# Kernel optimization log

Measured on AMD Instinct MI355X. Metric: run time of the kernel, lower is better.

The kernel has to match this reference:

```python
import jax, jax.numpy as jnp
import numpy as np

N_NODES = 50000
N_EDGES = 800000
N_GRAPHS = 256
F_IN, HID, EMB = 128, 256, 128
N_GROUPS, N_FAM = 16, 128


def setup_inputs() -> dict:
    key = jax.random.key(0)
    ks = jax.random.split(key, 12)
    x = jax.random.normal(ks[0], (N_NODES, F_IN), dtype=jnp.float32)
    edge_index = jax.random.randint(ks[1], (2, N_EDGES), 0, N_NODES, dtype=jnp.int64)
    batch = jnp.sort(jax.random.randint(ks[2], (N_NODES,), 0, N_GRAPHS, dtype=jnp.int64))
    def lin(k, fi, fo):
        s = 1.0 / np.sqrt(fi)
        return jax.random.uniform(k, (fi, fo), minval=-s, maxval=s, dtype=jnp.float32)
    W1 = lin(ks[3], F_IN, HID); b1 = jnp.zeros((HID,), jnp.float32)
    W2 = lin(ks[4], HID, EMB); b2 = jnp.zeros((EMB,), jnp.float32)
    Wg = lin(ks[5], EMB, N_GROUPS); bg = jnp.zeros((N_GROUPS,), jnp.float32)
    s = 1.0 / np.sqrt(EMB)
    Wf = jax.random.uniform(ks[6], (N_GROUPS, EMB, N_FAM), minval=-s, maxval=s, dtype=jnp.float32)
    bf = jnp.zeros((N_GROUPS, N_FAM), jnp.float32)
    return {"x": x, "edge_index": edge_index, "batch": batch,
            "W1": W1, "b1": b1, "W2": W2, "b2": b2,
            "Wg": Wg, "bg": bg, "Wf": Wf, "bf": bf}


def _gcn_conv(h, src, dst, coef, W, b, n):
    # h: [N, Fin]; src/dst: [E'] (self-loops included); coef: [E'] sym-norm
    hw = h @ W                                    # [N, Fout]
    msg = hw[src] * coef[:, None]                 # gather + scale, [E', Fout]
    out = jax.ops.segment_sum(msg, dst, num_segments=n)  # scatter-add
    return out + b


def reference(x, edge_index, batch, W1, b1, W2, b2, Wg, bg, Wf, bf):
    n = x.shape[0]
    loops = jnp.arange(n, dtype=edge_index.dtype)
    src = jnp.concatenate([edge_index[0], loops])
    dst = jnp.concatenate([edge_index[1], loops])
    # symmetric GCN normalization (deg >= 1 thanks to self-loops)
    deg = jax.ops.segment_sum(jnp.ones_like(dst, dtype=x.dtype), dst, num_segments=n)
    dinv = jax.lax.rsqrt(deg)
    coef = dinv[src] * dinv[dst]

    h1 = jax.nn.relu(_gcn_conv(x, src, dst, coef, W1, b1, n))  # dropout = identity (eval)
    h2 = _gcn_conv(h1, src, dst, coef, W2, b2, n)

    # global mean pool over graphs
    sums = jax.ops.segment_sum(h2, batch, num_segments=N_GRAPHS)
    cnts = jax.ops.segment_sum(jnp.ones((n,), x.dtype), batch, num_segments=N_GRAPHS)
    embeddings = sums / jnp.maximum(cnts, 1.0)[:, None]        # [G, EMB]

    group_logits = embeddings @ Wg + bg                        # [G, n_groups]
    pred_groups = jnp.argmax(group_logits, axis=1)             # routing
    # per-graph routed family classifier (dense equivalent of the dict outputs)
    family_logits = jnp.einsum('gd,gdf->gf', embeddings, Wf[pred_groups]) + bf[pred_groups]
    return embeddings, group_logits, family_logits
```

## Files before the change

kernel.cpp:

```cpp
#include <hip/hip_runtime.h>
#include <hip/hip_fp16.h>
#include <cstddef>
#include <cstdint>

static constexpr int NN   = 50000;
static constexpr int NE   = 800000;
static constexpr int NG   = 256;
static constexpr int FIN  = 128;
static constexpr int HID  = 256;
static constexpr int EMB  = 128;
static constexpr int NGRP = 16;
static constexpr int NFAM = 128;
static constexpr int NETOT = NE + NN;

static constexpr int SCAN_B  = 256;
static constexpr int SCAN_CH = (NN + SCAN_B - 1) / SCAN_B;

using bf16x8 = __attribute__((ext_vector_type(8))) short;
using f32x4  = __attribute__((ext_vector_type(4))) float;

__device__ __forceinline__ unsigned short f2bf(float f) {
    uint32_t u = __float_as_uint(f);
    u += 0x7FFFu + ((u >> 16) & 1u);
    return (unsigned short)(u >> 16);
}
__device__ __forceinline__ float bf2f(unsigned short u) {
    return __uint_as_float((uint32_t)u << 16);
}
__device__ __forceinline__ uint32_t pack_sw(int s, float w) {
    return (uint32_t)s | ((uint32_t)__half_as_ushort(__float2half(w)) << 16);
}
__device__ __forceinline__ void unpack_sw(uint32_t v, int& s, float& w) {
    s = (int)(v & 0xFFFFu);
    w = __half2float(__ushort_as_half((unsigned short)(v >> 16)));
}


__global__ void k_init_deg(int* __restrict__ degi, int n) {
    int i = blockIdx.x * blockDim.x + threadIdx.x;
    if (i < n) degi[i] = 1;
}

__global__ void k_count(const int* __restrict__ edst, int* __restrict__ degi, int e) {
    int i = blockIdx.x * blockDim.x + threadIdx.x;
    if (i < e) atomicAdd(degi + edst[i], 1);
}

__global__ void k_prep(const int* __restrict__ degi, const int* __restrict__ batch,
                       float* __restrict__ dinv, int* __restrict__ gstart,
                       float* __restrict__ pooled, int n, int G) {
    int i = blockIdx.x * blockDim.x + threadIdx.x;
    if (i < NG * HID) pooled[i] = 0.f;
    if (i >= n) return;
    dinv[i] = rsqrtf((float)degi[i]);
    int b  = batch[i];
    int pb = (i == 0) ? -1 : batch[i - 1];
    for (int g = pb + 1; g <= b; ++g) gstart[g] = i;
    if (i == n - 1) {
        for (int g = b + 1; g <= G; ++g) gstart[g] = n;
    }
}

__global__ void k_xconv(const float* __restrict__ x, unsigned short* __restrict__ xb) {
    size_t i = (size_t)(blockIdx.x * blockDim.x + threadIdx.x) * 8;
    float4 a = *(const float4*)(x + i);
    float4 b = *(const float4*)(x + i + 4);
    uint4 o;
    o.x = (uint32_t)f2bf(a.x) | ((uint32_t)f2bf(a.y) << 16);
    o.y = (uint32_t)f2bf(a.z) | ((uint32_t)f2bf(a.w) << 16);
    o.z = (uint32_t)f2bf(b.x) | ((uint32_t)f2bf(b.y) << 16);
    o.w = (uint32_t)f2bf(b.z) | ((uint32_t)f2bf(b.w) << 16);
    *(uint4*)(xb + i) = o;
}

__global__ void k_w1t(const float* __restrict__ W1, unsigned short* __restrict__ W1t) {
    int t = blockIdx.x * blockDim.x + threadIdx.x;
    int nidx = t >> 7, k = t & 127;
    W1t[t] = f2bf(W1[(size_t)k * HID + nidx]);
}


__global__ __launch_bounds__(256) void k_scanA(const int* __restrict__ degi,
                                               int* __restrict__ row_ptr,
                                               int* __restrict__ bsum, int n) {
    __shared__ int sh[256];
    const int b = blockIdx.x, t = threadIdx.x;
    const int idx = b * SCAN_CH + t;
    int v = 0;
    if (t < SCAN_CH && idx < n) v = degi[idx];
    sh[t] = v;
    __syncthreads();
    for (int off = 1; off < 256; off <<= 1) {
        int y = (t >= off) ? sh[t - off] : 0;
        __syncthreads();
        if (t >= off) sh[t] += y;
        __syncthreads();
    }
    if (t < SCAN_CH && idx < n) row_ptr[idx] = sh[t] - v;
    if (t == 255) bsum[b] = sh[255];
}

__global__ __launch_bounds__(256) void k_scanB(const int* __restrict__ bsum,
                                               const int* __restrict__ gstart,
                                               float* __restrict__ rcnt,
                                               int* __restrict__ row_ptr,
                                               int* __restrict__ cursor, int n) {
    __shared__ int sh[SCAN_B];
    const int b = blockIdx.x, t = threadIdx.x;
    sh[t] = bsum[t];
    __syncthreads();
    for (int off = 1; off < SCAN_B; off <<= 1) {
        int y = (t >= off) ? sh[t - off] : 0;
        __syncthreads();
        if (t >= off) sh[t] += y;
        __syncthreads();
    }
    const int boff = (b == 0) ? 0 : sh[b - 1];
    const int idx  = b * SCAN_CH + t;
    if (t < SCAN_CH && idx < n) {
        row_ptr[idx] += boff;
        cursor[idx] = 1;
    }
    if (b == 0 && t == 0) row_ptr[n] = sh[SCAN_B - 1];
    if (b == 0 && t < NG) {
        int c = gstart[t + 1] - gstart[t];
        rcnt[t] = 1.0f / (float)max(c, 1);
    }
}

__global__ void k_build(const int* __restrict__ esrc, const int* __restrict__ edst,
                        const int* __restrict__ batch, const float* __restrict__ dinv,
                        const float* __restrict__ rcnt, const int* __restrict__ row_ptr,
                        int* __restrict__ cursor, uint32_t* __restrict__ eA,
                        uint32_t* __restrict__ eP, int n, int e) {
    int i = blockIdx.x * blockDim.x + threadIdx.x;
    if (i < n) {
        int p = row_ptr[i];
        float di = dinv[i];
        eA[p] = pack_sw(i, di);
        eP[p] = pack_sw(i, di * di * rcnt[batch[i]]);
    } else if (i < n + e) {
        int ei = i - n;
        int d = edst[ei], s = esrc[ei];
        int p = atomicAdd(cursor + d, 1);
        int idx = row_ptr[d] + p;
        float ds = dinv[s];
        eA[idx] = pack_sw(s, ds);
        eP[idx] = pack_sw(s, dinv[d] * ds * rcnt[batch[d]]);
    }
}


__global__ __launch_bounds__(256) void k_agg(
        const unsigned short* __restrict__ xb, const int* __restrict__ row_ptr,
        const uint32_t* __restrict__ eA, const float* __restrict__ dinv,
        unsigned short* __restrict__ xa, int n) {
    int node = blockIdx.x * 4 + (threadIdx.x >> 6);
    if (node >= n) return;
    int lane = threadIdx.x & 63;
    int grp = lane >> 4, fl = lane & 15;
    float acc[8] = {};
    int beg = row_ptr[node], end = row_ptr[node + 1];
    for (int j = beg; j < end; j += 4) {
        int jj = j + grp;
        bool valid = jj < end;
        uint32_t ev = __builtin_nontemporal_load(eA + (valid ? jj : beg));
        int s; float w;
        unpack_sw(ev, s, w);
        if (!valid) w = 0.f;
        bf16x8 v = *(const bf16x8*)(xb + ((size_t)s << 7) + fl * 8);
#pragma unroll
        for (int k = 0; k < 8; ++k)
            acc[k] += w * bf2f((unsigned short)v[k]);
    }
#pragma unroll
    for (int k = 0; k < 8; ++k) {
        acc[k] += __shfl_xor(acc[k], 16);
        acc[k] += __shfl_xor(acc[k], 32);
    }
    if (lane < 16) {
        float di = dinv[node];
        uint4 o;
        o.x = (uint32_t)f2bf(di * acc[0]) | ((uint32_t)f2bf(di * acc[1]) << 16);
        o.y = (uint32_t)f2bf(di * acc[2]) | ((uint32_t)f2bf(di * acc[3]) << 16);
        o.z = (uint32_t)f2bf(di * acc[4]) | ((uint32_t)f2bf(di * acc[5]) << 16);
        o.w = (uint32_t)f2bf(di * acc[6]) | ((uint32_t)f2bf(di * acc[7]) << 16);
        *(uint4*)(xa + ((size_t)node << 7) + fl * 8) = o;
    }
}


__global__ __launch_bounds__(256) void k_gemm_mfma(
        const unsigned short* __restrict__ A, const unsigned short* __restrict__ Bt,
        const float* __restrict__ bias, unsigned short* __restrict__ C, int M) {
    const int m0 = blockIdx.x * 64;
    const int w  = threadIdx.x >> 6;
    const int l  = threadIdx.x & 63;
    const int lr = l & 15;
    const int lk = l >> 4;
    const int n0 = blockIdx.y * 64 + w * 16;

    f32x4 acc[4] = {};
#pragma unroll
    for (int ks = 0; ks < 4; ++ks) {
        const int k0 = ks * 32;
        bf16x8 bfr = *(const bf16x8*)(Bt + (size_t)(n0 + lr) * FIN + k0 + lk * 8);
#pragma unroll
        for (int mi = 0; mi < 4; ++mi) {
            int row = m0 + mi * 16 + lr;
            row = min(row, M - 1);
            bf16x8 afr = *(const bf16x8*)(A + ((size_t)row << 7) + k0 + lk * 8);
            acc[mi] = __builtin_amdgcn_mfma_f32_16x16x32_bf16(afr, bfr, acc[mi], 0, 0, 0);
        }
    }
    float b = bias[n0 + lr];
#pragma unroll
    for (int mi = 0; mi < 4; ++mi) {
#pragma unroll
        for (int r = 0; r < 4; ++r) {
            int row = m0 + mi * 16 + lk * 4 + r;
            if (row < M) {
                float v = fmaxf(acc[mi][r] + b, 0.f);
                C[(size_t)row * HID + n0 + lr] = f2bf(v);
            }
        }
    }
}


__global__ __launch_bounds__(256) void k_pool(
        const unsigned short* __restrict__ h1, const int* __restrict__ row_ptr,
        const int* __restrict__ gstart, const uint32_t* __restrict__ eP,
        float* __restrict__ pooled) {
    __shared__ float red[4][HID];
    const int g  = blockIdx.x >> 3;
    const int kb = blockIdx.x & 7;
    const int e0 = row_ptr[gstart[g]];
    const int e1 = row_ptr[gstart[g + 1]];
    const int len = e1 - e0;
    const int per = (len + 7) >> 3;
    const int s0  = e0 + kb * per;
    const int s1  = min(s0 + per, e1);
    const int lane = threadIdx.x & 63;
    const int wv   = threadIdx.x >> 6;
    const int half = lane >> 5, fl = lane & 31;

    float acc[8] = {};
    for (int j = s0 + wv * 2; j < s1; j += 8) {
        int jj = j + half;
        bool valid = jj < s1;
        uint32_t ev = __builtin_nontemporal_load(eP + (valid ? jj : s0));
        int s; float w;
        unpack_sw(ev, s, w);
        if (!valid) w = 0.f;
        bf16x8 v = *(const bf16x8*)(h1 + ((size_t)s << 8) + fl * 8);
#pragma unroll
        for (int k = 0; k < 8; ++k)
            acc[k] += w * bf2f((unsigned short)v[k]);
    }
#pragma unroll
    for (int k = 0; k < 8; ++k)
        acc[k] += __shfl_xor(acc[k], 32);
    if (lane < 32) {
#pragma unroll
        for (int k = 0; k < 8; ++k)
            red[wv][fl * 8 + k] = acc[k];
    }
    __syncthreads();
    int t = threadIdx.x;
    float v = red[0][t] + red[1][t] + red[2][t] + red[3][t];
    if (v != 0.f) atomicAdd(&pooled[g * HID + t], v);
}


__global__ __launch_bounds__(128) void k_head(const float* __restrict__ pooled,
                                              const float* __restrict__ W2,
                                              const float* __restrict__ b2,
                                              const float* __restrict__ Wg,
                                              const float* __restrict__ bg,
                                              const float* __restrict__ Wf,
                                              const float* __restrict__ bf,
                                              float* __restrict__ out_emb,
                                              float* __restrict__ out_gl,
                                              float* __restrict__ out_fl) {
    __shared__ float p[HID];
    __shared__ float e[EMB];
    __shared__ float gl[NGRP];
    __shared__ int ps;
    int g = blockIdx.x, c = threadIdx.x;
    for (int i = c; i < HID; i += 128) p[i] = pooled[(size_t)g * HID + i];
    __syncthreads();
    float a = b2[c];
    for (int k = 0; k < HID; ++k) a += p[k] * W2[(size_t)k * EMB + c];
    e[c] = a;
    out_emb[(size_t)g * EMB + c] = a;
    __syncthreads();
    if (c < NGRP) {
        float s = bg[c];
        for (int d = 0; d < EMB; ++d) s += e[d] * Wg[d * NGRP + c];
        gl[c] = s;
        out_gl[g * NGRP + c] = s;
    }
    __syncthreads();
    if (c == 0) {
        int bi = 0;
        float bv = gl[0];
        for (int t2 = 1; t2 < NGRP; ++t2)
            if (gl[t2] > bv) { bv = gl[t2]; bi = t2; }
        ps = bi;
    }
    __syncthreads();
    int pr = ps;
    float s = bf[pr * NFAM + c];
    for (int d = 0; d < EMB; ++d) s += e[d] * Wf[((size_t)pr * EMB + d) * NFAM + c];
    out_fl[g * NFAM + c] = s;
}


extern "C" void kernel_launch(void* const* d_in, const int* in_sizes, int n_in,
                              void* d_out, int out_size, void* d_ws, size_t ws_size,
                              hipStream_t stream) {
    const float* x   = (const float*)d_in[0];
    const int*   ei  = (const int*)d_in[1];
    const int*   bat = (const int*)d_in[2];
    const float* W1  = (const float*)d_in[3];
    const float* b1  = (const float*)d_in[4];
    const float* W2  = (const float*)d_in[5];
    const float* b2  = (const float*)d_in[6];
    const float* Wg  = (const float*)d_in[7];
    const float* bg  = (const float*)d_in[8];
    const float* Wf  = (const float*)d_in[9];
    const float* bf  = (const float*)d_in[10];

    float* out     = (float*)d_out;
    float* out_emb = out;
    float* out_gl  = out + (size_t)NG * EMB;
    float* out_fl  = out_gl + (size_t)NG * NGRP;

    char* w = (char*)d_ws;
    auto alloc = [&](size_t bytes) {
        char* p = w;
        w += (bytes + 255) & ~(size_t)255;
        return p;
    };
    int*            degi    = (int*)alloc((size_t)NN * 4);
    float*          dinv    = (float*)alloc((size_t)NN * 4);
    int*            row_ptr = (int*)alloc((size_t)(NN + 1) * 4);
    int*            cursor  = (int*)alloc((size_t)NN * 4);
    int*            bsum    = (int*)alloc((size_t)SCAN_B * 4);
    uint32_t*       eA      = (uint32_t*)alloc((size_t)NETOT * 4);
    uint32_t*       eP      = (uint32_t*)alloc((size_t)NETOT * 4);
    int*            gstart  = (int*)alloc((size_t)(NG + 1) * 4);
    float*          rcnt    = (float*)alloc((size_t)NG * 4);
    unsigned short* xb      = (unsigned short*)alloc((size_t)NN * FIN * 2);
    unsigned short* xa      = (unsigned short*)alloc((size_t)NN * FIN * 2);
    unsigned short* W1t     = (unsigned short*)alloc((size_t)HID * FIN * 2);
    unsigned short* h1      = (unsigned short*)alloc((size_t)NN * HID * 2);
    float*          pooled  = (float*)alloc((size_t)NG * HID * 4);

    const int* esrc = ei;
    const int* edst = ei + NE;

    k_init_deg<<<(NN + 255) / 256, 256, 0, stream>>>(degi, NN);
    k_count<<<(NE + 255) / 256, 256, 0, stream>>>(edst, degi, NE);
    k_prep<<<(NG * HID + 255) / 256, 256, 0, stream>>>(degi, bat, dinv, gstart,
                                                       pooled, NN, NG);
    k_xconv<<<(NN * FIN / 8 + 255) / 256, 256, 0, stream>>>(x, xb);
    k_w1t<<<(HID * FIN + 255) / 256, 256, 0, stream>>>(W1, W1t);
    k_scanA<<<SCAN_B, 256, 0, stream>>>(degi, row_ptr, bsum, NN);
    k_scanB<<<SCAN_B, 256, 0, stream>>>(bsum, gstart, rcnt, row_ptr, cursor, NN);
    k_build<<<(NETOT + 255) / 256, 256, 0, stream>>>(esrc, edst, bat, dinv, rcnt,
                                                     row_ptr, cursor, eA, eP, NN, NE);

    k_agg<<<(NN + 3) / 4, 256, 0, stream>>>(xb, row_ptr, eA, dinv, xa, NN);
    {
        dim3 grid((NN + 63) / 64, HID / 64);
        k_gemm_mfma<<<grid, 256, 0, stream>>>(xa, W1t, b1, h1, NN);
    }

    k_pool<<<NG * 8, 256, 0, stream>>>(h1, row_ptr, gstart, eP, pooled);

    k_head<<<NG, 128, 0, stream>>>(pooled, W2, b2, Wg, bg, Wf, bf,
                                   out_emb, out_gl, out_fl);
}
```

Baseline: 258.6 us.

## Fuse second GCN linear into first GEMM and pool over 128-wide features

The second layer's W2 projection now runs inside the first GEMM kernel: each 64-row block computes relu(xa@W1+b1), keeps it in swizzled LDS, multiplies by W2, and writes a 128-wide H. This replaces the 256-wide h1 intermediate and the per-graph W2 matvec in the head. The source-side dinv scaling is folded into x before aggregation and into H, so edge lists store only indices or dst-side weights. The trade-offs are an extra bf16 rounding of h1 before the second GEMM, 32KB of LDS per block that may limit occupancy, and a bias b2 that is added only for nonempty graphs.

```diff
diff --git a/kernel.cpp b/kernel.cpp
--- a/kernel.cpp
+++ b/kernel.cpp
@@ -48,9 +48,9 @@
 
 __global__ void k_prep(const int* __restrict__ degi, const int* __restrict__ batch,
                        float* __restrict__ dinv, int* __restrict__ gstart,
-                       float* __restrict__ pooled, int n, int G) {
+                       float* __restrict__ emb_acc, int n, int G) {
     int i = blockIdx.x * blockDim.x + threadIdx.x;
-    if (i < NG * HID) pooled[i] = 0.f;
+    if (i < NG * EMB) emb_acc[i] = 0.f;
     if (i >= n) return;
     dinv[i] = rsqrtf((float)degi[i]);
     int b  = batch[i];
@@ -61,22 +61,31 @@
     }
 }
 
-__global__ void k_xconv(const float* __restrict__ x, unsigned short* __restrict__ xb) {
-    size_t i = (size_t)(blockIdx.x * blockDim.x + threadIdx.x) * 8;
+__global__ void k_xconv(const float* __restrict__ x, const float* __restrict__ dinv,
+                        unsigned short* __restrict__ xs) {
+    int t = blockIdx.x * blockDim.x + threadIdx.x;
+    size_t i = (size_t)t * 8;
+    float dv = dinv[t >> 4];
     float4 a = *(const float4*)(x + i);
     float4 b = *(const float4*)(x + i + 4);
     uint4 o;
-    o.x = (uint32_t)f2bf(a.x) | ((uint32_t)f2bf(a.y) << 16);
-    o.y = (uint32_t)f2bf(a.z) | ((uint32_t)f2bf(a.w) << 16);
-    o.z = (uint32_t)f2bf(b.x) | ((uint32_t)f2bf(b.y) << 16);
-    o.w = (uint32_t)f2bf(b.z) | ((uint32_t)f2bf(b.w) << 16);
-    *(uint4*)(xb + i) = o;
+    o.x = (uint32_t)f2bf(dv * a.x) | ((uint32_t)f2bf(dv * a.y) << 16);
+    o.y = (uint32_t)f2bf(dv * a.z) | ((uint32_t)f2bf(dv * a.w) << 16);
+    o.z = (uint32_t)f2bf(dv * b.x) | ((uint32_t)f2bf(dv * b.y) << 16);
+    o.w = (uint32_t)f2bf(dv * b.z) | ((uint32_t)f2bf(dv * b.w) << 16);
+    *(uint4*)(xs + i) = o;
 }
 
 __global__ void k_w1t(const float* __restrict__ W1, unsigned short* __restrict__ W1t) {
     int t = blockIdx.x * blockDim.x + threadIdx.x;
     int nidx = t >> 7, k = t & 127;
     W1t[t] = f2bf(W1[(size_t)k * HID + nidx]);
+}
+
+__global__ void k_w2t(const float* __restrict__ W2, unsigned short* __restrict__ W2t) {
+    int t = blockIdx.x * blockDim.x + threadIdx.x;
+    int nidx = t >> 8, k = t & 255;
+    W2t[t] = f2bf(W2[(size_t)k * EMB + nidx]);
 }
 
 
@@ -131,29 +140,27 @@
 __global__ void k_build(const int* __restrict__ esrc, const int* __restrict__ edst,
                         const int* __restrict__ batch, const float* __restrict__ dinv,
                         const float* __restrict__ rcnt, const int* __restrict__ row_ptr,
-                        int* __restrict__ cursor, uint32_t* __restrict__ eA,
+                        int* __restrict__ cursor, int* __restrict__ eA,
                         uint32_t* __restrict__ eP, int n, int e) {
     int i = blockIdx.x * blockDim.x + threadIdx.x;
     if (i < n) {
         int p = row_ptr[i];
-        float di = dinv[i];
-        eA[p] = pack_sw(i, di);
-        eP[p] = pack_sw(i, di * di * rcnt[batch[i]]);
+        eA[p] = i;
+        eP[p] = pack_sw(i, dinv[i] * rcnt[batch[i]]);
     } else if (i < n + e) {
         int ei = i - n;
         int d = edst[ei], s = esrc[ei];
         int p = atomicAdd(cursor + d, 1);
         int idx = row_ptr[d] + p;
-        float ds = dinv[s];
-        eA[idx] = pack_sw(s, ds);
-        eP[idx] = pack_sw(s, dinv[d] * ds * rcnt[batch[d]]);
+        eA[idx] = s;
+        eP[idx] = pack_sw(s, dinv[d] * rcnt[batch[d]]);
     }
 }
 
 
 __global__ __launch_bounds__(256) void k_agg(
-        const unsigned short* __restrict__ xb, const int* __restrict__ row_ptr,
-        const uint32_t* __restrict__ eA, const float* __restrict__ dinv,
+        const unsigned short* __restrict__ xs, const int* __restrict__ row_ptr,
+        const int* __restrict__ eA, const float* __restrict__ dinv,
         unsigned short* __restrict__ xa, int n) {
     int node = blockIdx.x * 4 + (threadIdx.x >> 6);
     if (node >= n) return;
@@ -164,14 +171,12 @@
     for (int j = beg; j < end; j += 4) {
         int jj = j + grp;
         bool valid = jj < end;
-        uint32_t ev = __builtin_nontemporal_load(eA + (valid ? jj : beg));
-        int s; float w;
-        unpack_sw(ev, s, w);
-        if (!valid) w = 0.f;
-        bf16x8 v = *(const bf16x8*)(xb + ((size_t)s << 7) + fl * 8);
+        int s = __builtin_nontemporal_load(eA + (valid ? jj : beg));
+        float m = valid ? 1.f : 0.f;
+        bf16x8 v = *(const bf16x8*)(xs + ((size_t)s << 7) + fl * 8);
 #pragma unroll
         for (int k = 0; k < 8; ++k)
-            acc[k] += w * bf2f((unsigned short)v[k]);
+            acc[k] += m * bf2f((unsigned short)v[k]);
     }
 #pragma unroll
     for (int k = 0; k < 8; ++k) {
@@ -190,49 +195,109 @@
 }
 
 
-__global__ __launch_bounds__(256) void k_gemm_mfma(
-        const unsigned short* __restrict__ A, const unsigned short* __restrict__ Bt,
-        const float* __restrict__ bias, unsigned short* __restrict__ C, int M) {
+__global__ __launch_bounds__(256) void k_fgemm(
+        const unsigned short* __restrict__ A,
+        const unsigned short* __restrict__ W1t,
+        const unsigned short* __restrict__ W2t,
+        const float* __restrict__ b1, const float* __restrict__ dinv,
+        unsigned short* __restrict__ H, int M) {
+    __shared__ unsigned short h1s[64 * 256];
     const int m0 = blockIdx.x * 64;
     const int w  = threadIdx.x >> 6;
     const int l  = threadIdx.x & 63;
     const int lr = l & 15;
     const int lk = l >> 4;
-    const int n0 = blockIdx.y * 64 + w * 16;
-
-    f32x4 acc[4] = {};
-#pragma unroll
-    for (int ks = 0; ks < 4; ++ks) {
-        const int k0 = ks * 32;
-        bf16x8 bfr = *(const bf16x8*)(Bt + (size_t)(n0 + lr) * FIN + k0 + lk * 8);
-#pragma unroll
-        for (int mi = 0; mi < 4; ++mi) {
-            int row = m0 + mi * 16 + lr;
-            row = min(row, M - 1);
-            bf16x8 afr = *(const bf16x8*)(A + ((size_t)row << 7) + k0 + lk * 8);
-            acc[mi] = __builtin_amdgcn_mfma_f32_16x16x32_bf16(afr, bfr, acc[mi], 0, 0, 0);
-        }
-    }
-    float b = bias[n0 + lr];
-#pragma unroll
-    for (int mi = 0; mi < 4; ++mi) {
-#pragma unroll
-        for (int r = 0; r < 4; ++r) {
-            int row = m0 + mi * 16 + lk * 4 + r;
-            if (row < M) {
-                float v = fmaxf(acc[mi][r] + b, 0.f);
-                C[(size_t)row * HID + n0 + lr] = f2bf(v);
+
+    {
+        f32x4 acc[4][4] = {};
+        const int n0 = w * 64;
+#pragma unroll
+        for (int ks = 0; ks < 4; ++ks) {
+            const int k0 = ks * 32 + lk * 8;
+            bf16x8 bfr[4];
+#pragma unroll
+            for (int ni = 0; ni < 4; ++ni)
+                bfr[ni] = *(const bf16x8*)(W1t + (size_t)(n0 + ni * 16 + lr) * FIN + k0);
+#pragma unroll
+            for (int mi = 0; mi < 4; ++mi) {
+                int row = min(m0 + mi * 16 + lr, M - 1);
+                bf16x8 afr = *(const bf16x8*)(A + ((size_t)row << 7) + k0);
+#pragma unroll
+                for (int ni = 0; ni < 4; ++ni)
+                    acc[mi][ni] = __builtin_amdgcn_mfma_f32_16x16x32_bf16(
+                        afr, bfr[ni], acc[mi][ni], 0, 0, 0);
             }
         }
+#pragma unroll
+        for (int ni = 0; ni < 4; ++ni) {
+            int col = n0 + ni * 16 + lr;
+            float bb = b1[col];
+#pragma unroll
+            for (int mi = 0; mi < 4; ++mi) {
+#pragma unroll
+                for (int r = 0; r < 4; ++r) {
+                    int rl = mi * 16 + lk * 4 + r;
+                    float dv = dinv[min(m0 + rl, M - 1)];
+                    float v = fmaxf(acc[mi][ni][r] + bb, 0.f) * dv;
+                    int byte = (rl * 512 + col * 2) ^ ((rl & 7) << 4);
+                    *(unsigned short*)((char*)h1s + byte) = f2bf(v);
+                }
+            }
+        }
+    }
+    __syncthreads();
+    f32x4 acc2[4][2] = {};
+    {
+        const int n0 = w * 32;
+#pragma unroll
+        for (int ks = 0; ks < 8; ++ks) {
+            const int k0 = ks * 32 + lk * 8;
+            bf16x8 bfr[2];
+#pragma unroll
+            for (int ni = 0; ni < 2; ++ni)
+                bfr[ni] = *(const bf16x8*)(W2t + (size_t)(n0 + ni * 16 + lr) * HID + k0);
+#pragma unroll
+            for (int mi = 0; mi < 4; ++mi) {
+                int rl = mi * 16 + lr;
+                int byte = (rl * 512 + k0 * 2) ^ ((rl & 7) << 4);
+                bf16x8 afr = *(const bf16x8*)((const char*)h1s + byte);
+#pragma unroll
+                for (int ni = 0; ni < 2; ++ni)
+                    acc2[mi][ni] = __builtin_amdgcn_mfma_f32_16x16x32_bf16(
+                        afr, bfr[ni], acc2[mi][ni], 0, 0, 0);
+            }
+        }
+    }
+    __syncthreads();
+    {
+        const int n0 = w * 32;
+#pragma unroll
+        for (int ni = 0; ni < 2; ++ni) {
+            int col = n0 + ni * 16 + lr;
+#pragma unroll
+            for (int mi = 0; mi < 4; ++mi)
+#pragma unroll
+                for (int r = 0; r < 4; ++r) {
+                    int rl = mi * 16 + lk * 4 + r;
+                    h1s[rl * EMB + col] = f2bf(acc2[mi][ni][r]);
+                }
+        }
+    }
+    __syncthreads();
+    int nrows = min(64, M - m0);
+    for (int c = threadIdx.x; c < nrows * 16; c += 256) {
+        int rl = c >> 4, cc = c & 15;
+        *(uint4*)(H + ((size_t)(m0 + rl) << 7) + cc * 8) =
+            *(const uint4*)(h1s + rl * EMB + cc * 8);
     }
 }
 
 
 __global__ __launch_bounds__(256) void k_pool(
-        const unsigned short* __restrict__ h1, const int* __restrict__ row_ptr,
+        const unsigned short* __restrict__ H, const int* __restrict__ row_ptr,
         const int* __restrict__ gstart, const uint32_t* __restrict__ eP,
-        float* __restrict__ pooled) {
-    __shared__ float red[4][HID];
+        float* __restrict__ emb_acc) {
+    __shared__ float red[4][EMB];
     const int g  = blockIdx.x >> 3;
     const int kb = blockIdx.x & 7;
     const int e0 = row_ptr[gstart[g]];
@@ -243,55 +308,55 @@
     const int s1  = min(s0 + per, e1);
     const int lane = threadIdx.x & 63;
     const int wv   = threadIdx.x >> 6;
-    const int half = lane >> 5, fl = lane & 31;
+    const int grp = lane >> 4, fl = lane & 15;
 
     float acc[8] = {};
-    for (int j = s0 + wv * 2; j < s1; j += 8) {
-        int jj = j + half;
+    for (int j = s0 + wv * 4; j < s1; j += 16) {
+        int jj = j + grp;
         bool valid = jj < s1;
         uint32_t ev = __builtin_nontemporal_load(eP + (valid ? jj : s0));
-        int s; float w;
-        unpack_sw(ev, s, w);
-        if (!valid) w = 0.f;
-        bf16x8 v = *(const bf16x8*)(h1 + ((size_t)s << 8) + fl * 8);
+        int s; float wgt;
+        unpack_sw(ev, s, wgt);
+        if (!valid) wgt = 0.f;
+        bf16x8 v = *(const bf16x8*)(H + ((size_t)s << 7) + fl * 8);
 #pragma unroll
         for (int k = 0; k < 8; ++k)
-            acc[k] += w * bf2f((unsigned short)v[k]);
-    }
-#pragma unroll
-    for (int k = 0; k < 8; ++k)
+            acc[k] += wgt * bf2f((unsigned short)v[k]);
+    }
+#pragma unroll
+    for (int k = 0; k < 8; ++k) {
+        acc[k] += __shfl_xor(acc[k], 16);
         acc[k] += __shfl_xor(acc[k], 32);
-    if (lane < 32) {
-#pragma unroll
-        for (int k = 0; k < 8; ++k)
-            red[wv][fl * 8 + k] = acc[k];
+    }
+    if (lane < 16) {
+#pragma unroll
+        for (int k = 0; k < 8; ++k) red[wv][fl * 8 + k] = acc[k];
     }
     __syncthreads();
     int t = threadIdx.x;
-    float v = red[0][t] + red[1][t] + red[2][t] + red[3][t];
-    if (v != 0.f) atomicAdd(&pooled[g * HID + t], v);
-}
-
-
-__global__ __launch_bounds__(128) void k_head(const float* __restrict__ pooled,
-                                              const float* __restrict__ W2,
+    if (t < EMB) {
+        float v = red[0][t] + red[1][t] + red[2][t] + red[3][t];
+        if (v != 0.f) atomicAdd(&emb_acc[g * EMB + t], v);
+    }
+}
+
+
+__global__ __launch_bounds__(128) void k_head(const float* __restrict__ emb_acc,
+                                              const int* __restrict__ gstart,
                                               const float* __restrict__ b2,
                                               const float* __restrict__ Wg,
                                               const float* __restrict__ bg,
                                               const float* __restrict__ Wf,
-                                              const float* __restrict__ bf,
+                                              const float* __restrict__ bff,
                                               float* __restrict__ out_emb,
                                               float* __restrict__ out_gl,
                                               float* __restrict__ out_fl) {
-    __shared__ float p[HID];
     __shared__ float e[EMB];
     __shared__ float gl[NGRP];
     __shared__ int ps;
     int g = blockIdx.x, c = threadIdx.x;
-    for (int i = c; i < HID; i += 128) p[i] = pooled[(size_t)g * HID + i];
-    __syncthreads();
-    float a = b2[c];
-    for (int k = 0; k < HID; ++k) a += p[k] * W2[(size_t)k * EMB + c];
+    bool nonempty = gstart[g + 1] > gstart[g];
+    float a = emb_acc[g * EMB + c] + (nonempty ? b2[c] : 0.f);
     e[c] = a;
     out_emb[(size_t)g * EMB + c] = a;
     __syncthreads();
@@ -311,7 +376,7 @@
     }
     __syncthreads();
     int pr = ps;
-    float s = bf[pr * NFAM + c];
+    float s = bff[pr * NFAM + c];
     for (int d = 0; d < EMB; ++d) s += e[d] * Wf[((size_t)pr * EMB + d) * NFAM + c];
     out_fl[g * NFAM + c] = s;
 }
@@ -348,15 +413,16 @@
     int*            row_ptr = (int*)alloc((size_t)(NN + 1) * 4);
     int*            cursor  = (int*)alloc((size_t)NN * 4);
     int*            bsum    = (int*)alloc((size_t)SCAN_B * 4);
-    uint32_t*       eA      = (uint32_t*)alloc((size_t)NETOT * 4);
+    int*            eA      = (int*)alloc((size_t)NETOT * 4);
     uint32_t*       eP      = (uint32_t*)alloc((size_t)NETOT * 4);
     int*            gstart  = (int*)alloc((size_t)(NG + 1) * 4);
     float*          rcnt    = (float*)alloc((size_t)NG * 4);
-    unsigned short* xb      = (unsigned short*)alloc((size_t)NN * FIN * 2);
+    unsigned short* xs      = (unsigned short*)alloc((size_t)NN * FIN * 2);
     unsigned short* xa      = (unsigned short*)alloc((size_t)NN * FIN * 2);
     unsigned short* W1t     = (unsigned short*)alloc((size_t)HID * FIN * 2);
-    unsigned short* h1      = (unsigned short*)alloc((size_t)NN * HID * 2);
-    float*          pooled  = (float*)alloc((size_t)NG * HID * 4);
+    unsigned short* W2t     = (unsigned short*)alloc((size_t)EMB * HID * 2);
+    unsigned short* H       = (unsigned short*)alloc((size_t)NN * EMB * 2);
+    float*          emb_acc = (float*)alloc((size_t)NG * EMB * 4);
 
     const int* esrc = ei;
     const int* edst = ei + NE;
@@ -364,22 +430,20 @@
     k_init_deg<<<(NN + 255) / 256, 256, 0, stream>>>(degi, NN);
     k_count<<<(NE + 255) / 256, 256, 0, stream>>>(edst, degi, NE);
     k_prep<<<(NG * HID + 255) / 256, 256, 0, stream>>>(degi, bat, dinv, gstart,
-                                                       pooled, NN, NG);
-    k_xconv<<<(NN * FIN / 8 + 255) / 256, 256, 0, stream>>>(x, xb);
-    k_w1t<<<(HID * FIN + 255) / 256, 256, 0, stream>>>(W1, W1t);
+                                                       emb_acc, NN, NG);
+    k_xconv<<<(NN * 16) / 256, 256, 0, stream>>>(x, dinv, xs);
+    k_w1t<<<(HID * FIN) / 256, 256, 0, stream>>>(W1, W1t);
+    k_w2t<<<(EMB * HID) / 256, 256, 0, stream>>>(W2, W2t);
     k_scanA<<<SCAN_B, 256, 0, stream>>>(degi, row_ptr, bsum, NN);
     k_scanB<<<SCAN_B, 256, 0, stream>>>(bsum, gstart, rcnt, row_ptr, cursor, NN);
     k_build<<<(NETOT + 255) / 256, 256, 0, stream>>>(esrc, edst, bat, dinv, rcnt,
                                                      row_ptr, cursor, eA, eP, NN, NE);
 
-    k_agg<<<(NN + 3) / 4, 256, 0, stream>>>(xb, row_ptr, eA, dinv, xa, NN);
-    {
-        dim3 grid((NN + 63) / 64, HID / 64);
-        k_gemm_mfma<<<grid, 256, 0, stream>>>(xa, W1t, b1, h1, NN);
-    }
-
-    k_pool<<<NG * 8, 256, 0, stream>>>(h1, row_ptr, gstart, eP, pooled);
-
-    k_head<<<NG, 128, 0, stream>>>(pooled, W2, b2, Wg, bg, Wf, bf,
+    k_agg<<<(NN + 3) / 4, 256, 0, stream>>>(xs, row_ptr, eA, dinv, xa, NN);
+    k_fgemm<<<(NN + 63) / 64, 256, 0, stream>>>(xa, W1t, W2t, b1, dinv, H, NN);
+
+    k_pool<<<NG * 8, 256, 0, stream>>>(H, row_ptr, gstart, eP, emb_acc);
+
+    k_head<<<NG, 128, 0, stream>>>(emb_acc, gstart, b2, Wg, bg, Wf, bf,
                                    out_emb, out_gl, out_fl);
 }
```

Result: faster. 216.6 us (-16.2%).
